# Performance work log

Hardware: AMD Instinct MI355X
Metric: run time of the kernel (lower is better)

## Reference

```python
import jax, jax.numpy as jnp
import numpy as np


def setup_inputs() -> dict:
    key = jax.random.key(0)
    k1, k2, k3 = jax.random.split(key, 3)
    S, B, H = 4096, 16, 1024
    hidden = jax.random.normal(k1, (1, B, H), dtype=jnp.float32)
    encoder_outputs = jax.random.normal(k2, (S, B, H), dtype=jnp.float32)
    W_attn = jax.random.normal(k3, (H, H), dtype=jnp.float32) * (1.0 / np.sqrt(H))
    b_attn = jnp.zeros((H,), dtype=jnp.float32)
    return {"hidden": hidden, "encoder_outputs": encoder_outputs,
            "W_attn": W_attn, "b_attn": b_attn}


def reference(hidden, encoder_outputs, W_attn, b_attn):
    # method == 'general': energy_i = hidden_b . (W @ enc_{i,b} + b)
    # encoder_outputs: [S, B, H]; hidden: [1, B, H]
    proj = jnp.einsum('sbh,kh->sbk', encoder_outputs, W_attn) + b_attn  # [S,B,H]
    energies = jnp.einsum('bh,sbh->bs', hidden[0], proj)                # [B,S]
    attn = jax.nn.softmax(energies, axis=-1)
    return attn[:, None, :]  # [B, 1, S]
```

## Files before the change

### kernel.cpp

```cpp
#include <hip/hip_runtime.h>
#include <math.h>


#define SS 4096
#define BB 16
#define HH 1024
#define KC 16
#define KLEN (HH / KC)
#define PP 4

typedef float f4 __attribute__((ext_vector_type(4)));

__global__ void __launch_bounds__(256)
gemv_partial_kernel(const float* __restrict__ hidden,
                    const float* __restrict__ W,
                    float* __restrict__ partial) {
    int blk = blockIdx.x;
    int kc  = blk >> 6;
    int rb  = blk & 63;
    int b   = rb >> 2;
    int h   = ((rb & 3) << 8) | threadIdx.x;
    const float* hrow = hidden + b * HH + kc * KLEN;
    const float* Wp   = W + (size_t)(kc * KLEN) * HH + h;
    float a0 = 0.f, a1 = 0.f, a2 = 0.f, a3 = 0.f;
    #pragma unroll 4
    for (int k = 0; k < KLEN; k += 4) {
        a0 += hrow[k + 0] * Wp[(k + 0) * HH];
        a1 += hrow[k + 1] * Wp[(k + 1) * HH];
        a2 += hrow[k + 2] * Wp[(k + 2) * HH];
        a3 += hrow[k + 3] * Wp[(k + 3) * HH];
    }
    partial[kc * (BB * HH) + b * HH + h] = (a0 + a1) + (a2 + a3);
}

__global__ void __launch_bounds__(256)
gemv_reduce_kernel(const float* __restrict__ partial,
                   float* __restrict__ v) {
    int i = blockIdx.x * 256 + threadIdx.x;
    float s = 0.f;
    #pragma unroll
    for (int kc = 0; kc < KC; ++kc) s += partial[kc * (BB * HH) + i];
    v[i] = s;
}

__global__ void __launch_bounds__(256, 4)
energies_kernel(const float* __restrict__ enc,
                const float* __restrict__ v,
                float* __restrict__ out) {
    int w    = (blockIdx.x * blockDim.x + threadIdx.x) >> 6;
    int lane = threadIdx.x & 63;
    int b  = w & (BB - 1);
    int sg = w >> 4;
    const f4* v4 = (const f4*)(v + b * HH);
    f4 vv[4];
    #pragma unroll
    for (int i = 0; i < 4; ++i) vv[i] = v4[i * 64 + lane];
    float acc[PP];
    #pragma unroll
    for (int j = 0; j < PP; ++j) {
        const f4* e4 = (const f4*)(enc + (size_t)((sg * PP + j) * BB + b) * HH);
        f4 a0 = e4[0 * 64 + lane];
        f4 a1 = e4[1 * 64 + lane];
        f4 a2 = e4[2 * 64 + lane];
        f4 a3 = e4[3 * 64 + lane];
        f4 p  = a0 * vv[0] + a1 * vv[1] + a2 * vv[2] + a3 * vv[3];
        acc[j] = (p.x + p.y) + (p.z + p.w);
    }
    #pragma unroll
    for (int j = 0; j < PP; ++j) {
        #pragma unroll
        for (int off = 32; off; off >>= 1) acc[j] += __shfl_xor(acc[j], off, 64);
    }
    if (lane == 0) {
        f4 o;
        o.x = acc[0]; o.y = acc[1]; o.z = acc[2]; o.w = acc[3];
        *(f4*)(out + b * SS + sg * PP) = o;
    }
}

__global__ void __launch_bounds__(256)
softmax_kernel(float* __restrict__ out) {
    int b = blockIdx.x;
    float* row = out + b * SS;
    int t = threadIdx.x;
    float vals[16];
    float m = -INFINITY;
    #pragma unroll
    for (int i = 0; i < 16; ++i) {
        vals[i] = row[t + i * 256];
        m = fmaxf(m, vals[i]);
    }
    #pragma unroll
    for (int off = 32; off; off >>= 1) m = fmaxf(m, __shfl_xor(m, off, 64));
    __shared__ float redm[4];
    __shared__ float reds[4];
    int wid = t >> 6;
    if ((t & 63) == 0) redm[wid] = m;
    __syncthreads();
    m = fmaxf(fmaxf(redm[0], redm[1]), fmaxf(redm[2], redm[3]));

    float sum = 0.f;
    #pragma unroll
    for (int i = 0; i < 16; ++i) {
        vals[i] = expf(vals[i] - m);
        sum += vals[i];
    }
    #pragma unroll
    for (int off = 32; off; off >>= 1) sum += __shfl_xor(sum, off, 64);
    if ((t & 63) == 0) reds[wid] = sum;
    __syncthreads();
    sum = reds[0] + reds[1] + reds[2] + reds[3];
    float inv = 1.0f / sum;
    #pragma unroll
    for (int i = 0; i < 16; ++i) row[t + i * 256] = vals[i] * inv;
}

extern "C" void kernel_launch(void* const* d_in, const int* in_sizes, int n_in,
                              void* d_out, int out_size, void* d_ws, size_t ws_size,
                              hipStream_t stream) {
    const float* hidden = (const float*)d_in[0];
    const float* enc    = (const float*)d_in[1];
    const float* W      = (const float*)d_in[2];
    float* out     = (float*)d_out;
    float* v       = (float*)d_ws;
    float* partial = v + BB * HH;

    hipLaunchKernelGGL(gemv_partial_kernel, dim3(KC * 64), dim3(256), 0, stream,
                       hidden, W, partial);
    hipLaunchKernelGGL(gemv_reduce_kernel, dim3(BB * HH / 256), dim3(256), 0, stream,
                       partial, v);
    hipLaunchKernelGGL(energies_kernel, dim3(SS * BB / PP / 4), dim3(256), 0, stream,
                       enc, v, out);
    hipLaunchKernelGGL(softmax_kernel, dim3(BB), dim3(256), 0, stream, out);
}
```

Measured before the change: 57.22 us.

## Make energies kernel persistent with v cached in LDS

Replaces the one-shot energies grid with 512 persistent blocks of 512 threads. Each block stages the whole v matrix (64 KB) in shared memory, then loops over tiles of contiguous (s,b) rows, reading weights from LDS instead of global memory. This is meant to cut redundant global loads of v and the cost of launching many small blocks. In exchange, the 64 KB of LDS per block limits occupancy, and output writes become scattered scalar stores instead of f4 stores.

New measurement: 56.69 us. No clear change (-0.9%).

```diff
diff --git a/kernel.cpp b/kernel.cpp
--- a/kernel.cpp
+++ b/kernel.cpp
@@ -7,7 +7,11 @@
 #define HH 1024
 #define KC 16
 #define KLEN (HH / KC)
-#define PP 4
+
+#define BNB 512
+#define BNT 512
+#define NGRP (SS * BB / 32)
+#define TILES (NGRP / BNB)
 
 typedef float f4 __attribute__((ext_vector_type(4)));
 
@@ -43,38 +47,53 @@
     v[i] = s;
 }
 
-__global__ void __launch_bounds__(256, 4)
+__global__ void __launch_bounds__(BNT, 4)
 energies_kernel(const float* __restrict__ enc,
                 const float* __restrict__ v,
                 float* __restrict__ out) {
-    int w    = (blockIdx.x * blockDim.x + threadIdx.x) >> 6;
-    int lane = threadIdx.x & 63;
-    int b  = w & (BB - 1);
-    int sg = w >> 4;
-    const f4* v4 = (const f4*)(v + b * HH);
-    f4 vv[4];
+    __shared__ f4 vlds[BB * HH / 4];
+    int tid = threadIdx.x;
+    const f4* vg = (const f4*)v;
     #pragma unroll
-    for (int i = 0; i < 4; ++i) vv[i] = v4[i * 64 + lane];
-    float acc[PP];
-    #pragma unroll
-    for (int j = 0; j < PP; ++j) {
-        const f4* e4 = (const f4*)(enc + (size_t)((sg * PP + j) * BB + b) * HH);
-        f4 a0 = e4[0 * 64 + lane];
-        f4 a1 = e4[1 * 64 + lane];
-        f4 a2 = e4[2 * 64 + lane];
-        f4 a3 = e4[3 * 64 + lane];
-        f4 p  = a0 * vv[0] + a1 * vv[1] + a2 * vv[2] + a3 * vv[3];
-        acc[j] = (p.x + p.y) + (p.z + p.w);
-    }
-    #pragma unroll
-    for (int j = 0; j < PP; ++j) {
+    for (int it = 0; it < (BB * HH / 4) / BNT; ++it)
+        vlds[it * BNT + tid] = vg[it * BNT + tid];
+    __syncthreads();
+
+    int lane = tid & 63;
+    int wi   = tid >> 6;
+    for (int t = 0; t < TILES; ++t) {
+        int g  = t * BNB + blockIdx.x;
+        int p0 = g * 32 + wi * 4;
+        float acc[4];
         #pragma unroll
-        for (int off = 32; off; off >>= 1) acc[j] += __shfl_xor(acc[j], off, 64);
-    }
-    if (lane == 0) {
-        f4 o;
-        o.x = acc[0]; o.y = acc[1]; o.z = acc[2]; o.w = acc[3];
-        *(f4*)(out + b * SS + sg * PP) = o;
+        for (int j = 0; j < 4; ++j) {
+            int p = p0 + j;
+            int b = p & (BB - 1);
+            const f4* e4 = (const f4*)(enc + (size_t)p * HH);
+            f4 a0 = e4[0 * 64 + lane];
+            f4 a1 = e4[1 * 64 + lane];
+            f4 a2 = e4[2 * 64 + lane];
+            f4 a3 = e4[3 * 64 + lane];
+            f4 w0 = vlds[b * 256 + 0 * 64 + lane];
+            f4 w1 = vlds[b * 256 + 1 * 64 + lane];
+            f4 w2 = vlds[b * 256 + 2 * 64 + lane];
+            f4 w3 = vlds[b * 256 + 3 * 64 + lane];
+            f4 pr = a0 * w0 + a1 * w1 + a2 * w2 + a3 * w3;
+            acc[j] = (pr.x + pr.y) + (pr.z + pr.w);
+        }
+        #pragma unroll
+        for (int j = 0; j < 4; ++j) {
+            #pragma unroll
+            for (int off = 32; off; off >>= 1)
+                acc[j] += __shfl_xor(acc[j], off, 64);
+        }
+        if (lane == 0) {
+            #pragma unroll
+            for (int j = 0; j < 4; ++j) {
+                int p = p0 + j;
+                out[(p & (BB - 1)) * SS + (p >> 4)] = acc[j];
+            }
+        }
     }
 }
 
@@ -129,7 +148,7 @@
                        hidden, W, partial);
     hipLaunchKernelGGL(gemv_reduce_kernel, dim3(BB * HH / 256), dim3(256), 0, stream,
                        partial, v);
-    hipLaunchKernelGGL(energies_kernel, dim3(SS * BB / PP / 4), dim3(256), 0, stream,
+    hipLaunchKernelGGL(energies_kernel, dim3(BNB), dim3(BNT), 0, stream,
                        enc, v, out);
     hipLaunchKernelGGL(softmax_kernel, dim3(BB), dim3(256), 0, stream, out);
 }
```
